# Kernel optimization log

Measured on AMD Instinct MI355X. Metric: run time of the kernel, lower is better.

## Reference

```python
import jax, jax.numpy as jnp
import numpy as np

N = 8192
E_DIM = 256
HID = 256
OUT = 128
N_PRED = 2_000_000


def setup_inputs() -> dict:
    key = jax.random.key(0)
    ks = jax.random.split(key, 6)
    node_indices = jnp.arange(N, dtype=jnp.int64) if jax.config.jax_enable_x64 else jnp.arange(N, dtype=jnp.int32)
    attn_matrix = jax.random.normal(ks[0], (N, N), dtype=jnp.float32)
    edge_label_index = jax.random.randint(ks[1], (2, N_PRED), 0, N)
    emb = jax.random.normal(ks[2], (N, E_DIM), dtype=jnp.float32) * 0.05
    W1 = jax.random.normal(ks[3], (E_DIM, HID), dtype=jnp.float32) * (1.0 / np.sqrt(E_DIM))
    b1 = jnp.zeros((HID,), dtype=jnp.float32)
    W2 = jax.random.normal(ks[4], (HID, OUT), dtype=jnp.float32) * (1.0 / np.sqrt(HID))
    b2 = jnp.zeros((OUT,), dtype=jnp.float32)
    return {"node_indices": node_indices, "attn_matrix": attn_matrix,
            "edge_label_index": edge_label_index, "emb": emb,
            "W1": W1, "b1": b1, "W2": W2, "b2": b2}


def reference(node_indices, attn_matrix, edge_label_index, emb, W1, b1, W2, b2):
    # dense_to_sparse of an (almost surely) all-nonzero dense matrix keeps all
    # N^2 edges (incl. diagonal), so no extra self-loops are added by gcn_norm.
    w = jax.nn.relu(attn_matrix)                       # edge weights after F.relu
    deg = w.sum(axis=0)                                # deg[j] = sum_i w[i,j] (scatter on col)
    dis = jnp.where(deg > 0, jax.lax.rsqrt(deg), 0.0)  # deg^{-1/2}, inf -> 0
    a_norm = dis[:, None] * w * dis[None, :]           # norm_ij = d_i^-1/2 w_ij d_j^-1/2

    x = emb[node_indices]                              # embedding lookup [N, E_DIM]
    # GCNConv: aggregate transformed features at target (col): out = A_norm^T @ (x W) + b
    h = jax.nn.relu(a_norm.T @ (x @ W1) + b1)          # [N, HID]
    z = a_norm.T @ (h @ W2) + b2                       # [N, OUT]

    # decode: dot product between endpoint embeddings
    scores = jnp.einsum('ed,ed->e', z[edge_label_index[0]], z[edge_label_index[1]])
    return scores
```

## Files before the change

### kernel.cpp

```cpp
#include <hip/hip_runtime.h>

typedef _Float16 half8  __attribute__((ext_vector_type(8)));
typedef _Float16 half4v __attribute__((ext_vector_type(4)));
typedef _Float16 half2v __attribute__((ext_vector_type(2)));
typedef float    floatx4 __attribute__((ext_vector_type(4)));
typedef float    f4v     __attribute__((ext_vector_type(4)));

#define NND 8192
#define PA  40
#define PT  128

__device__ __forceinline__ int swzk(int m, int k) { return k ^ (((m >> 3) & 3) << 3); }
__device__ __forceinline__ int swzT(int row, int chunk) { return chunk ^ ((row >> 2) & 15); }

#define GLOAD16(gp, lp) __builtin_amdgcn_global_load_lds(                        \
    (const __attribute__((address_space(1))) void*)(gp),                         \
    (__attribute__((address_space(3))) void*)(lp), 16, 0, 0)

#define VMCNT0() asm volatile("s_waitcnt vmcnt(0)" ::: "memory")

__global__ __launch_bounds__(256) void k_degT(const float* __restrict__ A,
                                              _Float16* __restrict__ Wh,
                                              float* __restrict__ deg) {
    __shared__ _Float16 T[128 * PT];
    __shared__ float sdeg[8 * 128];
    int t  = threadIdx.x;
    int j0 = blockIdx.x * 128, i0 = blockIdx.y * 128;
    int c = t & 31;
    int g = t >> 5;

    f4v s = {0.f, 0.f, 0.f, 0.f};
    #pragma unroll
    for (int p = 0; p < 2; ++p) {
        int rb = 64 * p + 8 * g;
        f4v v[8];
        #pragma unroll
        for (int rr = 0; rr < 8; ++rr)
            v[rr] = *(const f4v*)(A + (size_t)(i0 + rb + rr) * NND + j0 + 4 * c);
        #pragma unroll
        for (int rr = 0; rr < 8; ++rr)
            #pragma unroll
            for (int u = 0; u < 4; ++u) v[rr][u] = fmaxf(v[rr][u], 0.f);
        #pragma unroll
        for (int u = 0; u < 4; ++u) {
            half8 hv;
            #pragma unroll
            for (int rr = 0; rr < 8; ++rr) { hv[rr] = (_Float16)v[rr][u]; s[u] += v[rr][u]; }
            int row = 4 * c + u;
            int chunk = 8 * p + g;
            *(half8*)(&T[row * PT + swzT(row, chunk) * 8]) = hv;
        }
    }
    *(f4v*)(&sdeg[g * 128 + 4 * c]) = s;
    __syncthreads();

    if (t < 128) {
        float d = 0.f;
        #pragma unroll
        for (int g2 = 0; g2 < 8; ++g2) d += sdeg[g2 * 128 + t];
        atomicAdd(&deg[j0 + t], d);
    }

    #pragma unroll
    for (int p = 0; p < 8; ++p) {
        int j  = 16 * p + (t >> 4);
        int mc = t & 15;
        half8 hv = *(const half8*)(&T[j * PT + swzT(j, mc) * 8]);
        *(half8*)(Wh + (size_t)(j0 + j) * NND + i0 + mc * 8) = hv;
    }
}

__global__ __launch_bounds__(256) void k_dis(const float* __restrict__ deg, float* __restrict__ dis) {
    int j = blockIdx.x * 256 + threadIdx.x;
    float d = deg[j];
    dis[j] = d > 0.f ? 1.f / sqrtf(d) : 0.f;
}

template <typename AT>
__global__ __launch_bounds__(256) void k_mm_small(
    const AT* __restrict__ Abase, const int* __restrict__ gather,
    const float* __restrict__ B, int NB,
    _Float16* __restrict__ outT, const float* __restrict__ dis, float out_scale) {

    __shared__ _Float16 As[128 * PA];
    __shared__ _Float16 Bs[64 * PA];

    int t  = threadIdx.x;
    int i0 = blockIdx.x * 128;
    int n0 = blockIdx.y * 64;

    int am = t & 127, akh = t >> 7;
    int row = i0 + am;
    if (gather) row = gather[row];
    const AT* arow = Abase + (size_t)row * 256;

    int tp = t & 15, kp = t >> 4;

    int lane = t & 63, w = t >> 6;
    int wm = w & 1, wn = w >> 1;
    int lm = lane & 15, q = lane >> 4;

    floatx4 acc[4][2];
    #pragma unroll
    for (int a = 0; a < 4; ++a)
        #pragma unroll
        for (int b = 0; b < 2; ++b) acc[a][b] = (floatx4){0.f, 0.f, 0.f, 0.f};

    for (int ks = 0; ks < 8; ++ks) {
        int c0 = ks * 32;

        half8 av[2];
        if constexpr (sizeof(AT) == 4) {
            #pragma unroll
            for (int cc = 0; cc < 2; ++cc) {
                f4v v0 = *(const f4v*)(arow + c0 + akh * 16 + cc * 8);
                f4v v1 = *(const f4v*)(arow + c0 + akh * 16 + cc * 8 + 4);
                half8 hv;
                #pragma unroll
                for (int e = 0; e < 4; ++e) {
                    hv[e]     = (_Float16)(16.f * v0[e]);
                    hv[4 + e] = (_Float16)(16.f * v1[e]);
                }
                av[cc] = hv;
            }
        } else {
            av[0] = *(const half8*)(arow + c0 + akh * 16);
            av[1] = *(const half8*)(arow + c0 + akh * 16 + 8);
        }

        const float* bp = B + (size_t)(c0 + 2 * kp) * NB + n0 + 4 * tp;
        f4v r0 = *(const f4v*)bp;
        f4v r1 = *(const f4v*)(bp + NB);

        __syncthreads();
        #pragma unroll
        for (int cc = 0; cc < 2; ++cc) {
            int k = akh * 16 + cc * 8;
            *(half8*)(&As[am * PA + swzk(am, k)]) = av[cc];
        }
        #pragma unroll
        for (int u = 0; u < 4; ++u) {
            int n = 4 * tp + u;
            half2v p = {(_Float16)r0[u], (_Float16)r1[u]};
            *(half2v*)(&Bs[n * PA + swzk(n, 2 * kp)]) = p;
        }
        __syncthreads();

        half8 af[4], bf[2];
        #pragma unroll
        for (int mt = 0; mt < 4; ++mt) {
            int m = wm * 64 + mt * 16 + lm;
            af[mt] = *(const half8*)(&As[m * PA + swzk(m, q * 8)]);
        }
        #pragma unroll
        for (int nt = 0; nt < 2; ++nt) {
            int n = wn * 32 + nt * 16 + lm;
            bf[nt] = *(const half8*)(&Bs[n * PA + swzk(n, q * 8)]);
        }
        #pragma unroll
        for (int mt = 0; mt < 4; ++mt)
            #pragma unroll
            for (int nt = 0; nt < 2; ++nt)
                acc[mt][nt] = __builtin_amdgcn_mfma_f32_16x16x32_f16(af[mt], bf[nt], acc[mt][nt], 0, 0, 0);
    }

    #pragma unroll
    for (int mt = 0; mt < 4; ++mt) {
        int ib = i0 + wm * 64 + mt * 16 + q * 4;
        #pragma unroll
        for (int nt = 0; nt < 2; ++nt) {
            int n = n0 + wn * 32 + nt * 16 + lm;
            #pragma unroll
            for (int r = 0; r < 4; ++r) {
                float v = acc[mt][nt][r] * dis[ib + r] * out_scale;
                outT[(size_t)n * NND + ib + r] = (_Float16)v;
            }
        }
    }
}

template <int BN, int ZSTEPS>
__global__ __launch_bounds__(256) void k_mm_big(
    const _Float16* __restrict__ Wh, const _Float16* __restrict__ Bt, float* __restrict__ Cp) {

    __shared__ __align__(16) _Float16 As[2 * 128 * 32];
    __shared__ __align__(16) _Float16 Bs[2 * 128 * 32];

    int t = threadIdx.x;
    int j0 = blockIdx.x * 128;
    int n0 = blockIdx.y * 128;
    size_t i_begin = (size_t)blockIdx.z * (ZSTEPS * 32);
    float* C = Cp + (size_t)blockIdx.z * (size_t)NND * BN;

    int lane = t & 63, w = t >> 6;
    int wm = w & 1, wn = w >> 1;
    int lm = lane & 15, q = lane >> 4;

    int srow = lane >> 2;
    int scol = (lane & 3) * 8;
    const _Float16* aS0 = Wh + (size_t)(j0 + w * 16 + srow) * NND + i_begin + scol;
    const _Float16* aS1 = aS0 + (size_t)64 * NND;
    const _Float16* bS0 = Bt + (size_t)(n0 + w * 16 + srow) * NND + i_begin + scol;
    const _Float16* bS1 = bS0 + (size_t)64 * NND;

    char* aLb = (char*)As + w * 1024;
    char* bLb = (char*)Bs + w * 1024;

    floatx4 acc[4][4];
    #pragma unroll
    for (int a = 0; a < 4; ++a)
        #pragma unroll
        for (int b = 0; b < 4; ++b) acc[a][b] = (floatx4){0.f, 0.f, 0.f, 0.f};

    {
        GLOAD16(aS0, aLb);
        GLOAD16(aS1, aLb + 4096);
        GLOAD16(bS0, bLb);
        GLOAD16(bS1, bLb + 4096);
    }
    VMCNT0();
    __builtin_amdgcn_s_barrier();

    for (int ks = 0; ks < ZSTEPS; ++ks) {
        int cur = ks & 1;
        const _Float16* Ab = As + cur * 4096;
        const _Float16* Bb = Bs + cur * 4096;

        if (ks < ZSTEPS - 1) {
            int ko = (ks + 1) * 32;
            char* aL = aLb + (cur ^ 1) * 8192;
            char* bL = bLb + (cur ^ 1) * 8192;
            GLOAD16(aS0 + ko, aL);
            GLOAD16(aS1 + ko, aL + 4096);
            GLOAD16(bS0 + ko, bL);
            GLOAD16(bS1 + ko, bL + 4096);
        }

        half8 af[4], bf[4];
        #pragma unroll
        for (int mt = 0; mt < 4; ++mt) {
            int m = wm * 64 + mt * 16 + lm;
            af[mt] = *(const half8*)(&Ab[m * 32 + q * 8]);
        }
        #pragma unroll
        for (int nt = 0; nt < 4; ++nt) {
            int n = wn * 64 + nt * 16 + lm;
            bf[nt] = *(const half8*)(&Bb[n * 32 + q * 8]);
        }
        __builtin_amdgcn_s_setprio(1);
        #pragma unroll
        for (int mt = 0; mt < 4; ++mt)
            #pragma unroll
            for (int nt = 0; nt < 4; ++nt)
                acc[mt][nt] = __builtin_amdgcn_mfma_f32_16x16x32_f16(af[mt], bf[nt], acc[mt][nt], 0, 0, 0);
        __builtin_amdgcn_s_setprio(0);

        VMCNT0();
        __builtin_amdgcn_s_barrier();
    }

    #pragma unroll
    for (int mt = 0; mt < 4; ++mt) {
        int rb = j0 + wm * 64 + mt * 16 + q * 4;
        #pragma unroll
        for (int nt = 0; nt < 4; ++nt) {
            int col = n0 + wn * 64 + nt * 16 + lm;
            #pragma unroll
            for (int r = 0; r < 4; ++r)
                C[(size_t)(rb + r) * BN + col] = acc[mt][nt][r];
        }
    }
}

template <int NSH, bool RELU, int NZ>
__global__ __launch_bounds__(256) void k_finalize(const float* __restrict__ Cp, const float* __restrict__ dis,
                                                  const float* __restrict__ bias, _Float16* __restrict__ out) {
    int idx4 = (blockIdx.x * 256 + threadIdx.x) * 4;
    f4v v = {0.f, 0.f, 0.f, 0.f};
    #pragma unroll
    for (int z = 0; z < NZ; ++z) {
        f4v p = *(const f4v*)(Cp + (size_t)z * (NND << NSH) + idx4);
        #pragma unroll
        for (int r = 0; r < 4; ++r) v[r] += p[r];
    }
    int j  = idx4 >> NSH;
    int n0 = idx4 & ((1 << NSH) - 1);
    float dj = dis[j] * (1.f / 1024.f);
    f4v b4 = *(const f4v*)(bias + n0);
    half4v o;
    #pragma unroll
    for (int r = 0; r < 4; ++r) {
        float x = v[r] * dj + b4[r];
        if (RELU) x = fmaxf(x, 0.f);
        o[r] = (_Float16)(x * 64.f);
    }
    *(half4v*)(out + idx4) = o;
}

__global__ __launch_bounds__(256) void k_edges(const _Float16* __restrict__ zh, const int* __restrict__ ei,
                                               float* __restrict__ out, int npred) {
    int g0 = ((blockIdx.x * 256 + threadIdx.x) >> 4) * 4;
    int l = threadIdx.x & 15;
    #pragma unroll
    for (int e = 0; e < 4; ++e) {
        int g = g0 + e;
        if (g >= npred) return;
        int a = ei[g], b = ei[npred + g];
        half8 za = *(const half8*)(zh + (size_t)a * 128 + l * 8);
        half8 zb = *(const half8*)(zh + (size_t)b * 128 + l * 8);
        float s = 0.f;
        #pragma unroll
        for (int u = 0; u < 4; ++u) {
            half2v a2 = {za[2 * u], za[2 * u + 1]};
            half2v b2 = {zb[2 * u], zb[2 * u + 1]};
            s = __builtin_amdgcn_fdot2(a2, b2, s, false);
        }
        s += __shfl_xor(s, 1);
        s += __shfl_xor(s, 2);
        s += __shfl_xor(s, 4);
        s += __shfl_xor(s, 8);
        if (l == 0) out[g] = s * (1.f / 4096.f);
    }
}

extern "C" void kernel_launch(void* const* d_in, const int* in_sizes, int n_in,
                              void* d_out, int out_size, void* d_ws, size_t ws_size,
                              hipStream_t stream) {
    const int*   nodes = (const int*)d_in[0];
    const float* attn  = (const float*)d_in[1];
    const int*   eidx  = (const int*)d_in[2];
    const float* emb   = (const float*)d_in[3];
    const float* W1    = (const float*)d_in[4];
    const float* b1    = (const float*)d_in[5];
    const float* W2    = (const float*)d_in[6];
    const float* b2    = (const float*)d_in[7];
    float* out = (float*)d_out;
    int npred = in_sizes[2] / 2;

    char* ws = (char*)d_ws;
    float*    deg = (float*)(ws);
    float*    dis = (float*)(ws + 0x8000);
    _Float16* Wh  = (_Float16*)(ws + 0x10000);
    float*    C1p = (float*)(ws + 0x8010000);
    float*    C2p = (float*)(ws + 0xC010000);
    _Float16* M1p = (_Float16*)(ws + 0xE010000);
    _Float16* h   = (_Float16*)(ws + 0xE410000);
    _Float16* M2p = (_Float16*)(ws + 0xE810000);
    _Float16* zh  = (_Float16*)(ws + 0xEA10000);

    hipMemsetAsync(deg, 0, 8192 * sizeof(float), stream);

    k_degT<<<dim3(64, 64), 256, 0, stream>>>(attn, Wh, deg);
    k_dis<<<32, 256, 0, stream>>>(deg, dis);

    k_mm_small<float><<<dim3(64, 4), 256, 0, stream>>>(emb, nodes, W1, 256, M1p, dis, 64.f);
    k_mm_big<256, 64><<<dim3(64, 2, 4), 256, 0, stream>>>(Wh, M1p, C1p);
    k_finalize<8, true, 4><<<2048, 256, 0, stream>>>(C1p, dis, b1, h);
    k_mm_small<_Float16><<<dim3(64, 2), 256, 0, stream>>>(h, nullptr, W2, 128, M2p, dis, 16.f);
    k_mm_big<128, 32><<<dim3(64, 1, 8), 256, 0, stream>>>(Wh, M2p, C2p);
    k_finalize<7, false, 8><<<1024, 256, 0, stream>>>(C2p, dis, b2, zh);

    k_edges<<<(npred + 63) / 64, 256, 0, stream>>>(zh, eidx, out, npred);
}
```

Baseline: 605.2 us.

## Fuse rsqrt into consumers, swizzle big-GEMM LDS tiles and remap block order

Removes the separate k_dis kernel and computes deg^-1/2 inline inside k_mm_small and k_finalize, saving one launch. In k_mm_big, the global-to-LDS load columns and the matching MFMA fragment reads are XOR-swizzled so LDS reads hit fewer bank conflicts. The block x index is also permuted, likely to improve L2/cache locality across concurrently scheduled blocks. The added cost is recomputing the reciprocal square root redundantly in many threads.

```diff
diff --git a/kernel.cpp b/kernel.cpp
--- a/kernel.cpp
+++ b/kernel.cpp
@@ -18,6 +18,8 @@
     (__attribute__((address_space(3))) void*)(lp), 16, 0, 0)
 
 #define VMCNT0() asm volatile("s_waitcnt vmcnt(0)" ::: "memory")
+
+__device__ __forceinline__ float dis_of(float d) { return d > 0.f ? 1.f / sqrtf(d) : 0.f; }
 
 __global__ __launch_bounds__(256) void k_degT(const float* __restrict__ A,
                                               _Float16* __restrict__ Wh,
@@ -70,17 +72,11 @@
     }
 }
 
-__global__ __launch_bounds__(256) void k_dis(const float* __restrict__ deg, float* __restrict__ dis) {
-    int j = blockIdx.x * 256 + threadIdx.x;
-    float d = deg[j];
-    dis[j] = d > 0.f ? 1.f / sqrtf(d) : 0.f;
-}
-
 template <typename AT>
 __global__ __launch_bounds__(256) void k_mm_small(
     const AT* __restrict__ Abase, const int* __restrict__ gather,
     const float* __restrict__ B, int NB,
-    _Float16* __restrict__ outT, const float* __restrict__ dis, float out_scale) {
+    _Float16* __restrict__ outT, const float* __restrict__ deg, float out_scale) {
 
     __shared__ _Float16 As[128 * PA];
     __shared__ _Float16 Bs[64 * PA];
@@ -167,12 +163,15 @@
     #pragma unroll
     for (int mt = 0; mt < 4; ++mt) {
         int ib = i0 + wm * 64 + mt * 16 + q * 4;
+        float di[4];
+        #pragma unroll
+        for (int r = 0; r < 4; ++r) di[r] = dis_of(deg[ib + r]) * out_scale;
         #pragma unroll
         for (int nt = 0; nt < 2; ++nt) {
             int n = n0 + wn * 32 + nt * 16 + lm;
             #pragma unroll
             for (int r = 0; r < 4; ++r) {
-                float v = acc[mt][nt][r] * dis[ib + r] * out_scale;
+                float v = acc[mt][nt][r] * di[r];
                 outT[(size_t)n * NND + ib + r] = (_Float16)v;
             }
         }
@@ -187,7 +186,9 @@
     __shared__ __align__(16) _Float16 Bs[2 * 128 * 32];
 
     int t = threadIdx.x;
-    int j0 = blockIdx.x * 128;
+    int bx = blockIdx.x;
+    bx = (bx & 7) * 8 + (bx >> 3);
+    int j0 = bx * 128;
     int n0 = blockIdx.y * 128;
     size_t i_begin = (size_t)blockIdx.z * (ZSTEPS * 32);
     float* C = Cp + (size_t)blockIdx.z * (size_t)NND * BN;
@@ -195,9 +196,10 @@
     int lane = t & 63, w = t >> 6;
     int wm = w & 1, wn = w >> 1;
     int lm = lane & 15, q = lane >> 4;
+    int qa = q ^ ((lm >> 1) & 3);
 
     int srow = lane >> 2;
-    int scol = (lane & 3) * 8;
+    int scol = ((lane & 3) ^ ((lane >> 3) & 3)) * 8;
     const _Float16* aS0 = Wh + (size_t)(j0 + w * 16 + srow) * NND + i_begin + scol;
     const _Float16* aS1 = aS0 + (size_t)64 * NND;
     const _Float16* bS0 = Bt + (size_t)(n0 + w * 16 + srow) * NND + i_begin + scol;
@@ -212,12 +214,10 @@
         #pragma unroll
         for (int b = 0; b < 4; ++b) acc[a][b] = (floatx4){0.f, 0.f, 0.f, 0.f};
 
-    {
-        GLOAD16(aS0, aLb);
-        GLOAD16(aS1, aLb + 4096);
-        GLOAD16(bS0, bLb);
-        GLOAD16(bS1, bLb + 4096);
-    }
+    GLOAD16(aS0, aLb);
+    GLOAD16(aS1, aLb + 4096);
+    GLOAD16(bS0, bLb);
+    GLOAD16(bS1, bLb + 4096);
     VMCNT0();
     __builtin_amdgcn_s_barrier();
 
@@ -240,12 +240,12 @@
         #pragma unroll
         for (int mt = 0; mt < 4; ++mt) {
             int m = wm * 64 + mt * 16 + lm;
-            af[mt] = *(const half8*)(&Ab[m * 32 + q * 8]);
+            af[mt] = *(const half8*)(&Ab[m * 32 + qa * 8]);
         }
         #pragma unroll
         for (int nt = 0; nt < 4; ++nt) {
             int n = wn * 64 + nt * 16 + lm;
-            bf[nt] = *(const half8*)(&Bb[n * 32 + q * 8]);
+            bf[nt] = *(const half8*)(&Bb[n * 32 + qa * 8]);
         }
         __builtin_amdgcn_s_setprio(1);
         #pragma unroll
@@ -273,7 +273,7 @@
 }
 
 template <int NSH, bool RELU, int NZ>
-__global__ __launch_bounds__(256) void k_finalize(const float* __restrict__ Cp, const float* __restrict__ dis,
+__global__ __launch_bounds__(256) void k_finalize(const float* __restrict__ Cp, const float* __restrict__ deg,
                                                   const float* __restrict__ bias, _Float16* __restrict__ out) {
     int idx4 = (blockIdx.x * 256 + threadIdx.x) * 4;
     f4v v = {0.f, 0.f, 0.f, 0.f};
@@ -285,7 +285,7 @@
     }
     int j  = idx4 >> NSH;
     int n0 = idx4 & ((1 << NSH) - 1);
-    float dj = dis[j] * (1.f / 1024.f);
+    float dj = dis_of(deg[j]) * (1.f / 1024.f);
     f4v b4 = *(const f4v*)(bias + n0);
     half4v o;
     #pragma unroll
@@ -339,7 +339,6 @@
 
     char* ws = (char*)d_ws;
     float*    deg = (float*)(ws);
-    float*    dis = (float*)(ws + 0x8000);
     _Float16* Wh  = (_Float16*)(ws + 0x10000);
     float*    C1p = (float*)(ws + 0x8010000);
     float*    C2p = (float*)(ws + 0xC010000);
@@ -351,14 +350,13 @@
     hipMemsetAsync(deg, 0, 8192 * sizeof(float), stream);
 
     k_degT<<<dim3(64, 64), 256, 0, stream>>>(attn, Wh, deg);
-    k_dis<<<32, 256, 0, stream>>>(deg, dis);
-
-    k_mm_small<float><<<dim3(64, 4), 256, 0, stream>>>(emb, nodes, W1, 256, M1p, dis, 64.f);
+
+    k_mm_small<float><<<dim3(64, 4), 256, 0, stream>>>(emb, nodes, W1, 256, M1p, deg, 64.f);
     k_mm_big<256, 64><<<dim3(64, 2, 4), 256, 0, stream>>>(Wh, M1p, C1p);
-    k_finalize<8, true, 4><<<2048, 256, 0, stream>>>(C1p, dis, b1, h);
-    k_mm_small<_Float16><<<dim3(64, 2), 256, 0, stream>>>(h, nullptr, W2, 128, M2p, dis, 16.f);
+    k_finalize<8, true, 4><<<2048, 256, 0, stream>>>(C1p, deg, b1, h);
+    k_mm_small<_Float16><<<dim3(64, 2), 256, 0, stream>>>(h, nullptr, W2, 128, M2p, deg, 16.f);
     k_mm_big<128, 32><<<dim3(64, 1, 8), 256, 0, stream>>>(Wh, M2p, C2p);
-    k_finalize<7, false, 8><<<1024, 256, 0, stream>>>(C2p, dis, b2, zh);
+    k_finalize<7, false, 8><<<1024, 256, 0, stream>>>(C2p, deg, b2, zh);
 
     k_edges<<<(npred + 63) / 64, 256, 0, stream>>>(zh, eidx, out, npred);
 }
```

New measurement: 607.5 us. About the same (+0.4%).
